# Kernel optimization log

Hardware: AMD Instinct MI355X
Metric: run time of the kernel (lower is better)

## Reference

```python
import jax, jax.numpy as jnp
import numpy as np

K_TOP = 10  # module init k


def setup_inputs() -> dict:
    key = jax.random.key(0)
    k1, k2 = jax.random.split(key)
    B, C, H, W = 32, 512, 64, 64
    num_item = 100
    x = jax.random.normal(k1, (B, C, H, W), dtype=jnp.float32)
    # mempool initialized uniform(-stdv, stdv) with stdv = 1/sqrt(dim), as in init_memory
    stdv = 1.0 / np.sqrt(C)
    mempool = jax.random.uniform(k2, (num_item, C), minval=-stdv, maxval=stdv, dtype=jnp.float32)
    return {"x": x, "mempool": mempool}


def reference(x, mempool):
    B, C, H, W = x.shape
    # permute to channels-last, flatten spatial+batch -> queries [N, C]
    q = x.transpose(0, 2, 3, 1).reshape(-1, C)
    # attention over memory items: F.linear(query, mempool) == q @ mempool.T
    att = jax.nn.softmax(q @ mempool.T, axis=1)  # [N, num_item]
    val, idx = jax.lax.top_k(att, K_TOP)          # [N, k]
    val = jax.nn.softmax(val, axis=1)             # renormalize over top-k
    N = q.shape[0]
    # scatter renormalized weights back into a sparse attention matrix
    att_sp = jnp.zeros_like(att).at[jnp.arange(N)[:, None], idx].set(val)
    # reconstruct: F.linear(att, mempool.T) == att @ mempool
    out = (att_sp @ mempool).reshape(B, H, W, C).transpose(0, 3, 1, 2)
    # diversity loss on the memory pool
    m = mempool.shape[0]
    cosim = (mempool @ mempool.T) * 0.5
    off_diag = cosim * (1.0 - jnp.eye(m, dtype=cosim.dtype))
    loss = jnp.mean(jnp.abs(off_diag))
    return (out, loss)
```

## Files before the change

### kernel.cpp

```cpp
#include <hip/hip_runtime.h>
#include <math.h>

#define NITEM 100
#define CDIM 512
#define HW 4096
#define KTOP 10

typedef __attribute__((ext_vector_type(8))) short bf16x8;
typedef __attribute__((ext_vector_type(4))) float f32x4;

__device__ inline unsigned short bf16u(float f) {
  unsigned int u = __float_as_uint(f);
  u += 0x7fffu + ((u >> 16) & 1u);
  return (unsigned short)(u >> 16);
}

__global__ __launch_bounds__(256, 3) void logits_topk(
    const float* __restrict__ x, const float* __restrict__ mp,
    unsigned short* __restrict__ Wd)
{
  __shared__ float qs[32 * 128];
  __shared__ float ms[32 * 128];

  const int t   = threadIdx.x;
  const int tc  = t & 15;
  const int trg = t >> 4;
  const int n0  = blockIdx.x * 128;
  const int b   = n0 >> 12;
  const int sp0 = n0 & (HW - 1);
  const float* xb = x + (size_t)b * CDIM * HW + sp0;

  const int item = t & 127;
  const int half = t >> 7;
  const float* mrow = mp + (size_t)(item < NITEM ? item : 0) * CDIM + 16 * half;

  float acc[8][7];
  #pragma unroll
  for (int r = 0; r < 8; ++r)
    #pragma unroll
    for (int j = 0; j < 7; ++j) acc[r][j] = 0.f;

  float4 qv[4], mv4[4];
  #pragma unroll
  for (int j = 0; j < 4; ++j) {
    int task = t + 256 * j;
    int kk = task >> 5, c4 = (task & 31) << 2;
    qv[j] = *(const float4*)(xb + (size_t)kk * HW + c4);
  }
  #pragma unroll
  for (int u = 0; u < 4; ++u) mv4[u] = *(const float4*)(mrow + 4 * u);

  #pragma unroll 1
  for (int kt = 0; kt < 16; ++kt) {
    #pragma unroll
    for (int j = 0; j < 4; ++j)
      *(float4*)(qs + 4 * (t + 256 * j)) = qv[j];
    #pragma unroll
    for (int u = 0; u < 4; ++u) {
      ms[(16 * half + 4 * u + 0) * 128 + item] = mv4[u].x;
      ms[(16 * half + 4 * u + 1) * 128 + item] = mv4[u].y;
      ms[(16 * half + 4 * u + 2) * 128 + item] = mv4[u].z;
      ms[(16 * half + 4 * u + 3) * 128 + item] = mv4[u].w;
    }
    __syncthreads();
    if (kt < 15) {
      const int k0n = (kt + 1) * 32;
      #pragma unroll
      for (int j = 0; j < 4; ++j) {
        int task = t + 256 * j;
        int kk = task >> 5, c4 = (task & 31) << 2;
        qv[j] = *(const float4*)(xb + (size_t)(k0n + kk) * HW + c4);
      }
      #pragma unroll
      for (int u = 0; u < 4; ++u) mv4[u] = *(const float4*)(mrow + k0n + 4 * u);
    }
    #pragma unroll 2
    for (int kk = 0; kk < 32; ++kk) {
      const float* qr = qs + kk * 128 + 8 * trg;
      const float* mr = ms + kk * 128 + tc;
      float4 qa = *(const float4*)(qr);
      float4 qb = *(const float4*)(qr + 4);
      float mm[7] = {mr[0], mr[16], mr[32], mr[48], mr[64], mr[80], mr[96]};
      float qq[8] = {qa.x, qa.y, qa.z, qa.w, qb.x, qb.y, qb.z, qb.w};
      #pragma unroll
      for (int r = 0; r < 8; ++r)
        #pragma unroll
        for (int j = 0; j < 7; ++j)
          acc[r][j] = __builtin_fmaf(qq[r], mm[j], acc[r][j]);
    }
    __syncthreads();
  }

  const int baserow = n0 + 8 * trg;
  #pragma unroll
  for (int r = 0; r < 8; ++r) {
    float attv[KTOP]; int id[KTOP];
    float mx = 0.f, Z = 0.f;
    #pragma unroll
    for (int s = 0; s < KTOP; ++s) {
      float bv = -INFINITY; int bi = 0x7fffffff;
      #pragma unroll
      for (int j = 0; j < 7; ++j) {
        bool valid = (j < 6) || (tc < 4);
        float v = valid ? acc[r][j] : -INFINITY;
        if (v > bv) { bv = v; bi = tc + 16 * j; }
      }
      #pragma unroll
      for (int d = 1; d < 16; d <<= 1) {
        float ov = __shfl_xor(bv, d, 16);
        int   oi = __shfl_xor(bi, d, 16);
        if (ov > bv || (ov == bv && oi < bi)) { bv = ov; bi = oi; }
      }
      if (s == 0) {
        mx = bv;
        float zp = 0.f;
        #pragma unroll
        for (int j = 0; j < 7; ++j) {
          bool valid = (j < 6) || (tc < 4);
          zp += valid ? __expf(acc[r][j] - mx) : 0.f;
        }
        #pragma unroll
        for (int d = 1; d < 16; d <<= 1) zp += __shfl_xor(zp, d, 16);
        Z = zp;
      }
      attv[s] = bv; id[s] = bi;
      #pragma unroll
      for (int j = 0; j < 7; ++j)
        if (bi == tc + 16 * j) acc[r][j] = -INFINITY;
    }
    float invZ = 1.f / Z;
    float p0 = invZ;
    float s2 = 0.f, wv[KTOP];
    #pragma unroll
    for (int s = 0; s < KTOP; ++s) {
      float p = __expf(attv[s] - mx) * invZ;
      float e = __expf(p - p0);
      wv[s] = e; s2 += e;
    }
    float inv2 = 1.f / s2;
    unsigned short wb[KTOP];
    #pragma unroll
    for (int s = 0; s < KTOP; ++s) wb[s] = bf16u(wv[s] * inv2);
    unsigned int packed[4];
    #pragma unroll
    for (int q2 = 0; q2 < 4; ++q2) {
      unsigned int lo = 0u, hi = 0u;
      #pragma unroll
      for (int s = 0; s < KTOP; ++s) {
        lo = (id[s] == 8 * tc + 2 * q2)     ? (unsigned int)wb[s] : lo;
        hi = (id[s] == 8 * tc + 2 * q2 + 1) ? (unsigned int)wb[s] : hi;
      }
      packed[q2] = lo | (hi << 16);
    }
    if (tc < 14) {
      uint4 o; o.x = packed[0]; o.y = packed[1]; o.z = packed[2]; o.w = packed[3];
      *(uint4*)(Wd + (size_t)(baserow + r) * 112 + 8 * tc) = o;
    }
  }
}

__global__ __launch_bounds__(256, 2) void recon(
    const float* __restrict__ mp, const unsigned short* __restrict__ Wd,
    float* __restrict__ out)
{
  __shared__ unsigned short Ash[128 * 136];
  __shared__ unsigned short Bsh[128 * 136];
  const int t  = threadIdx.x;
  const int ct = blockIdx.x & 3, nt = blockIdx.x >> 2;
  const int c0 = ct * 128, n0 = nt * 128;
  const int b  = n0 >> 12, sp0 = n0 & (HW - 1);

  #pragma unroll
  for (int j = 0; j < 13; ++j) {
    int task = t + 256 * j;
    if (task < 3200) {
      int k = task >> 5, c4 = (task & 31) << 2;
      float4 v = *(const float4*)(mp + (size_t)k * CDIM + c0 + c4);
      Ash[(c4 + 0) * 136 + k] = bf16u(v.x);
      Ash[(c4 + 1) * 136 + k] = bf16u(v.y);
      Ash[(c4 + 2) * 136 + k] = bf16u(v.z);
      Ash[(c4 + 3) * 136 + k] = bf16u(v.w);
    }
  }
  {
    int c = t >> 1, hf = t & 1;
    unsigned int* A32 = (unsigned int*)Ash;
    #pragma unroll
    for (int j = 0; j < 9; ++j) { int k = 100 + 2 * (hf * 9 + j); A32[(c * 136 + k) >> 1] = 0u; }
  }
  {
    int n = t >> 1, hf = t & 1;
    #pragma unroll
    for (int j = 0; j < 7; ++j) {
      int f = hf * 7 + j;
      *(bf16x8*)(Bsh + n * 136 + 8 * f) = *(const bf16x8*)(Wd + (size_t)(n0 + n) * 112 + 8 * f);
    }
    unsigned int* B32 = (unsigned int*)Bsh;
    #pragma unroll
    for (int j = 0; j < 6; ++j) { int k = 112 + 2 * (hf * 6 + j); B32[(n * 136 + k) >> 1] = 0u; }
  }
  __syncthreads();

  const int w = t >> 6, l = t & 63;
  const int arow = l & 15, kg = l >> 4;
  f32x4 acc[2][8];
  #pragma unroll
  for (int cr = 0; cr < 2; ++cr)
    #pragma unroll
    for (int n = 0; n < 8; ++n) acc[cr][n] = (f32x4){0.f, 0.f, 0.f, 0.f};

  #pragma unroll
  for (int ks = 0; ks < 4; ++ks) {
    bf16x8 a0 = *(bf16x8*)(Ash + ((2 * w + 0) * 16 + arow) * 136 + ks * 32 + kg * 8);
    bf16x8 a1 = *(bf16x8*)(Ash + ((2 * w + 1) * 16 + arow) * 136 + ks * 32 + kg * 8);
    #pragma unroll
    for (int nn = 0; nn < 8; ++nn) {
      bf16x8 bb = *(bf16x8*)(Bsh + (nn * 16 + arow) * 136 + ks * 32 + kg * 8);
      acc[0][nn] = __builtin_amdgcn_mfma_f32_16x16x32_bf16(a0, bb, acc[0][nn], 0, 0, 0);
      acc[1][nn] = __builtin_amdgcn_mfma_f32_16x16x32_bf16(a1, bb, acc[1][nn], 0, 0, 0);
    }
  }

  float* ob = out + (size_t)b * CDIM * HW + sp0;
  #pragma unroll
  for (int cr = 0; cr < 2; ++cr) {
    #pragma unroll
    for (int nn = 0; nn < 8; ++nn) {
      int ncol = nn * 16 + arow;
      #pragma unroll
      for (int j = 0; j < 4; ++j) {
        int cc = c0 + (2 * w + cr) * 16 + kg * 4 + j;
        ob[(size_t)cc * HW + ncol] = acc[cr][nn][j];
      }
    }
  }
}

__global__ void loss_partial(const float* __restrict__ mp, float* __restrict__ part)
{
  __shared__ float mi[CDIM];
  __shared__ float red[4];
  const int i = blockIdx.x;
  const int t = threadIdx.x;
  for (int k = t; k < CDIM; k += 256) mi[k] = mp[i * CDIM + k];
  __syncthreads();
  float v = 0.f;
  if (t < NITEM && t != i) {
    const float* mj = mp + t * CDIM;
    float d = 0.f;
    #pragma unroll 8
    for (int k = 0; k < CDIM; ++k) d += mi[k] * mj[k];
    v = fabsf(0.5f * d);
  }
  #pragma unroll
  for (int o = 32; o > 0; o >>= 1) v += __shfl_down(v, o, 64);
  if ((t & 63) == 0) red[t >> 6] = v;
  __syncthreads();
  if (t == 0) part[i] = red[0] + red[1] + red[2] + red[3];
}

__global__ void loss_final(const float* __restrict__ part, float* __restrict__ out_loss)
{
  if (threadIdx.x == 0) {
    float s = 0.f;
    for (int i = 0; i < NITEM; ++i) s += part[i];
    *out_loss = s / (float)(NITEM * NITEM);
  }
}

extern "C" void kernel_launch(void* const* d_in, const int* in_sizes, int n_in,
                              void* d_out, int out_size, void* d_ws, size_t ws_size,
                              hipStream_t stream) {
  const float* x  = (const float*)d_in[0];
  const float* mp = (const float*)d_in[1];
  float* out = (float*)d_out;
  unsigned short* Wd = (unsigned short*)d_ws;
  float* part = (float*)((char*)d_ws + (size_t)131072 * 112 * 2);

  logits_topk<<<1024, 256, 0, stream>>>(x, mp, Wd);
  recon<<<4096, 256, 0, stream>>>(mp, Wd, out);
  loss_partial<<<NITEM, 256, 0, stream>>>(mp, part);
  loss_final<<<1, 64, 0, stream>>>(part, out + (out_size - 1));
}
```

Measured before the change: 386.9 us.

## Double-buffer query tiles via direct global-to-LDS async loads

Replaces the register-staged query tile loads with __builtin_amdgcn_global_load_lds, which writes straight into a double-buffered LDS tile. The next tile is fetched while the current one is consumed. This removes the register round trip and the LDS store instructions, and frees VGPRs. It raises LDS use per block from 32 KB to 48 KB. The launch-bounds hint is also replaced by an explicit amdgpu_waves_per_eu(3,3), which could constrain occupancy.

```diff
diff --git a/kernel.cpp b/kernel.cpp
--- a/kernel.cpp
+++ b/kernel.cpp
@@ -15,11 +15,12 @@
   return (unsigned short)(u >> 16);
 }
 
-__global__ __launch_bounds__(256, 3) void logits_topk(
+__global__ __launch_bounds__(256) __attribute__((amdgpu_waves_per_eu(3, 3)))
+void logits_topk(
     const float* __restrict__ x, const float* __restrict__ mp,
     unsigned short* __restrict__ Wd)
 {
-  __shared__ float qs[32 * 128];
+  __shared__ float qs[2][32 * 128];
   __shared__ float ms[32 * 128];
 
   const int t   = threadIdx.x;
@@ -30,31 +31,37 @@
   const int sp0 = n0 & (HW - 1);
   const float* xb = x + (size_t)b * CDIM * HW + sp0;
 
+  const int w = t >> 6, l = t & 63;
   const int item = t & 127;
   const int half = t >> 7;
   const float* mrow = mp + (size_t)(item < NITEM ? item : 0) * CDIM + 16 * half;
 
+  auto issue_q = [&](int kt, int buf) {
+    const int k0 = kt * 32;
+    #pragma unroll
+    for (int i = 0; i < 4; ++i) {
+      const float* src = xb + (size_t)(k0 + 8 * w + 2 * i + (l >> 5)) * HW + (l & 31) * 4;
+      float* dst = &qs[buf][(8 * w + 2 * i) * 128];
+      __builtin_amdgcn_global_load_lds(
+          (const __attribute__((address_space(1))) void*)src,
+          (__attribute__((address_space(3))) void*)dst, 16, 0, 0);
+    }
+  };
+
   float acc[8][7];
   #pragma unroll
   for (int r = 0; r < 8; ++r)
     #pragma unroll
     for (int j = 0; j < 7; ++j) acc[r][j] = 0.f;
 
-  float4 qv[4], mv4[4];
-  #pragma unroll
-  for (int j = 0; j < 4; ++j) {
-    int task = t + 256 * j;
-    int kk = task >> 5, c4 = (task & 31) << 2;
-    qv[j] = *(const float4*)(xb + (size_t)kk * HW + c4);
-  }
+  issue_q(0, 0);
+  float4 mv4[4];
   #pragma unroll
   for (int u = 0; u < 4; ++u) mv4[u] = *(const float4*)(mrow + 4 * u);
 
+  int buf = 0;
   #pragma unroll 1
   for (int kt = 0; kt < 16; ++kt) {
-    #pragma unroll
-    for (int j = 0; j < 4; ++j)
-      *(float4*)(qs + 4 * (t + 256 * j)) = qv[j];
     #pragma unroll
     for (int u = 0; u < 4; ++u) {
       ms[(16 * half + 4 * u + 0) * 128 + item] = mv4[u].x;
@@ -64,19 +71,15 @@
     }
     __syncthreads();
     if (kt < 15) {
+      issue_q(kt + 1, buf ^ 1);
       const int k0n = (kt + 1) * 32;
       #pragma unroll
-      for (int j = 0; j < 4; ++j) {
-        int task = t + 256 * j;
-        int kk = task >> 5, c4 = (task & 31) << 2;
-        qv[j] = *(const float4*)(xb + (size_t)(k0n + kk) * HW + c4);
-      }
-      #pragma unroll
       for (int u = 0; u < 4; ++u) mv4[u] = *(const float4*)(mrow + k0n + 4 * u);
     }
+    const float* qsb = qs[buf];
     #pragma unroll 2
     for (int kk = 0; kk < 32; ++kk) {
-      const float* qr = qs + kk * 128 + 8 * trg;
+      const float* qr = qsb + kk * 128 + 8 * trg;
       const float* mr = ms + kk * 128 + tc;
       float4 qa = *(const float4*)(qr);
       float4 qb = *(const float4*)(qr + 4);
@@ -89,6 +92,7 @@
           acc[r][j] = __builtin_fmaf(qq[r], mm[j], acc[r][j]);
     }
     __syncthreads();
+    buf ^= 1;
   }
 
   const int baserow = n0 + 8 * trg;
```

New measurement: 374.2 us (median of 2 runs). 1.03x faster.
